# Kernel tuning notes

Hardware: AMD Instinct MI355X
Metric: run time of the kernel (lower is better)

## Reference

```python
import jax, jax.numpy as jnp
import numpy as np

N = 100000   # nodes
R = 6        # relations (edge types)
E = 400000   # edges per relation
F_IN = 128   # metapath2vec embedding dim
HID = 128    # hidden_dim (conv1 out == conv2 out in RGCN)
OUT = 2      # out_size


def setup_inputs() -> dict:
    key = jax.random.key(0)
    ks = jax.random.split(key, 9)
    x = jax.random.normal(ks[0], (N, F_IN), dtype=jnp.float32)
    edge_src = jax.random.randint(ks[1], (R, E), 0, N, dtype=jnp.int32)
    edge_dst = jax.random.randint(ks[2], (R, E), 0, N, dtype=jnp.int32)
    W1 = jax.random.normal(ks[3], (R, F_IN, HID), dtype=jnp.float32) * 0.05
    b1 = jnp.zeros((R, HID), dtype=jnp.float32)
    W2 = jax.random.normal(ks[4], (R, HID, HID), dtype=jnp.float32) * 0.05
    b2 = jnp.zeros((R, HID), dtype=jnp.float32)
    Wc = jax.random.normal(ks[5], (HID, OUT), dtype=jnp.float32) * 0.05
    bc = jnp.zeros((OUT,), dtype=jnp.float32)
    return {"x": x, "edge_src": edge_src, "edge_dst": edge_dst,
            "W1": W1, "b1": b1, "W2": W2, "b2": b2, "Wc": Wc, "bc": bc}


def _graph_conv(x, src, dst, W, b):
    """DGL GraphConv, norm='both': D_dst^{-1/2} A D_src^{-1/2} X W + b."""
    ones = jnp.ones(src.shape, x.dtype)
    deg_out = jax.ops.segment_sum(ones, src, num_segments=N)  # [N]
    deg_in = jax.ops.segment_sum(ones, dst, num_segments=N)   # [N]
    norm_src = jnp.where(deg_out > 0, jax.lax.rsqrt(jnp.maximum(deg_out, 1.0)), 0.0)
    norm_dst = jnp.where(deg_in > 0, jax.lax.rsqrt(jnp.maximum(deg_in, 1.0)), 0.0)
    msg = (x * norm_src[:, None])[src]                         # [E, F] gather
    agg = jax.ops.segment_sum(msg, dst, num_segments=N)       # [N, F] scatter-sum
    return (agg * norm_dst[:, None]) @ W + b                  # [N, H]


def _hetero_layer(x, edge_src, edge_dst, W, b):
    # HeteroGraphConv(aggregate='sum'): run each relation's GraphConv, sum results.
    conv = jax.vmap(_graph_conv, in_axes=(None, 0, 0, 0, 0))
    return conv(x, edge_src, edge_dst, W, b).sum(axis=0)      # [N, H]


def reference(x, edge_src, edge_dst, W1, b1, W2, b2, Wc, bc):
    h = jax.nn.relu(_hetero_layer(x, edge_src, edge_dst, W1, b1))
    h = _hetero_layer(h, edge_src, edge_dst, W2, b2)
    g = h.mean(axis=0)          # mean-pool node embeddings -> graph embedding
    return g @ Wc + bc          # classifier logits, shape [OUT]
```

## Files before the change

### kernel.cpp

```cpp
#include <hip/hip_runtime.h>

#define N_NODES 100000
#define NREL 6
#define NEDGE 400000
#define FDIM 128
#define HID 128

constexpr int RN = NREL * N_NODES;
constexpr int NBIN = 391;
constexpr int BINCAP = 1280;
constexpr int CSRCAP = 2304;
constexpr int CHUNK = 8192;
constexpr int NCHUNK = (NEDGE + CHUNK - 1) / CHUNK;

constexpr int NB_XC = (N_NODES * 32) / 256;
constexpr int NB_WC = (NREL * FDIM * HID) / 256;
constexpr int PREP_BLOCKS = NB_XC + NB_WC + NREL + 1;

typedef __attribute__((ext_vector_type(8))) short short8;
typedef __attribute__((ext_vector_type(4))) float f32x4;

__device__ __forceinline__ unsigned short f2bf(float f) {
  union { float f; unsigned int u; } v; v.f = f;
  unsigned int u = v.u;
  unsigned int r = (u + 0x7FFFu + ((u >> 16) & 1u)) >> 16;
  return (unsigned short)r;
}
__device__ __forceinline__ float bflo(unsigned int w) {
  union { unsigned int u; float f; } v; v.u = w << 16; return v.f;
}
__device__ __forceinline__ float bfhi(unsigned int w) {
  union { unsigned int u; float f; } v; v.u = w & 0xffff0000u; return v.f;
}

__global__ void k_zero(unsigned int* __restrict__ p, int nwords) {
  int id = blockIdx.x * blockDim.x + threadIdx.x;
  if (id < nwords) p[id] = 0u;
}

__global__ __launch_bounds__(256) void k_phase1(
    const int* __restrict__ src, const int* __restrict__ dst,
    int* __restrict__ gCurIn, int* __restrict__ gCurOut,
    unsigned int* __restrict__ stIn, unsigned int* __restrict__ stOut) {
  __shared__ int hIn[NBIN], hOut[NBIN], bIn[NBIN], bOut[NBIN];
  const int r = blockIdx.x / NCHUNK;
  const int c = blockIdx.x % NCHUNK;
  const int t = threadIdx.x;
  for (int i = t; i < NBIN; i += 256) { hIn[i] = 0; hOut[i] = 0; }
  __syncthreads();
  const int base = c * CHUNK;
  const int lim = min(CHUNK, NEDGE - base);
  const int* __restrict__ sR = src + r * NEDGE + base;
  const int* __restrict__ dR = dst + r * NEDGE + base;
  for (int i = t; i < lim; i += 256) {
    atomicAdd(&hIn[dR[i] >> 8], 1);
    atomicAdd(&hOut[sR[i] >> 8], 1);
  }
  __syncthreads();
  for (int i = t; i < NBIN; i += 256) {
    bIn[i]  = atomicAdd(&gCurIn[r * NBIN + i], hIn[i]);
    bOut[i] = atomicAdd(&gCurOut[r * NBIN + i], hOut[i]);
    hIn[i] = 0; hOut[i] = 0;
  }
  __syncthreads();
  for (int i = t; i < lim; i += 256) {
    const int s = sR[i], d = dR[i];
    const int bi = d >> 8, bo = s >> 8;
    const int pi = bIn[bi] + atomicAdd(&hIn[bi], 1);
    const int po = bOut[bo] + atomicAdd(&hOut[bo], 1);
    if (pi < BINCAP)
      stIn[(size_t)(r * NBIN + bi) * BINCAP + pi] = ((unsigned)(d & 255) << 17) | (unsigned)s;
    if (po < BINCAP)
      stOut[(size_t)(r * NBIN + bo) * BINCAP + po] = ((unsigned)(s & 255) << 17) | (unsigned)d;
  }
}

__global__ __launch_bounds__(256) void k_p2a(const unsigned int* __restrict__ stOut,
                                             const int* __restrict__ gCurOut,
                                             float* __restrict__ ns) {
  __shared__ int cnt[256];
  const int rb = blockIdx.x;
  const int r = rb / NBIN, b = rb % NBIN;
  const int t = threadIdx.x;
  cnt[t] = 0;
  __syncthreads();
  const int m = min(gCurOut[rb], BINCAP);
  const unsigned int* __restrict__ st = stOut + (size_t)rb * BINCAP;
  for (int i = t; i < m; i += 256) atomicAdd(&cnt[st[i] >> 17], 1);
  __syncthreads();
  const int n = b * 256 + t;
  if (n < N_NODES) ns[r * N_NODES + n] = cnt[t] > 0 ? rsqrtf((float)cnt[t]) : 0.f;
}

__global__ __launch_bounds__(256) void k_p2in(const unsigned int* __restrict__ stIn,
                                              const int* __restrict__ gCurIn,
                                              const float* __restrict__ ns,
                                              int4* __restrict__ meta,
                                              float* __restrict__ ndA,
                                              int2* __restrict__ csr) {
  __shared__ int cnt[256], offs[256];
  __shared__ int wsum[4];
  const int rb = blockIdx.x;
  const int r = rb / NBIN, b = rb % NBIN;
  const int t = threadIdx.x;
  cnt[t] = 0;
  __syncthreads();
  const int m = min(gCurIn[rb], BINCAP);
  const unsigned int* __restrict__ st = stIn + (size_t)rb * BINCAP;
  for (int i = t; i < m; i += 256) atomicAdd(&cnt[st[i] >> 17], 1);
  __syncthreads();
  const int lane = t & 63, wid = t >> 6;
  const int pc = (cnt[t] + 3) & ~3;
  int sum = pc;
#pragma unroll
  for (int o = 1; o < 64; o <<= 1) {
    int y = __shfl_up(sum, o);
    if (lane >= o) sum += y;
  }
  if (lane == 63) wsum[wid] = sum;
  __syncthreads();
  int wadd = 0;
  for (int w = 0; w < wid; ++w) wadd += wsum[w];
  offs[t] = sum - pc + wadd;
  __syncthreads();
  const int n = b * 256 + t;
  const int binBase = rb * CSRCAP;
  if (n < N_NODES) {
    const int d = cnt[t];
    const float nd = d > 0 ? rsqrtf((float)d) : 0.f;
    meta[r * N_NODES + n] = make_int4(d, binBase + offs[t], __float_as_int(nd), 0);
    ndA[r * N_NODES + n] = nd;
    int2* __restrict__ c = csr + binBase + offs[t];
    for (int e = d; e < ((d + 3) & ~3); ++e) c[e] = make_int2(0, 0);
  }
  __syncthreads();
  cnt[t] = 0;
  __syncthreads();
  const float* __restrict__ nsr = ns + r * N_NODES;
  for (int i = t; i < m; i += 256) {
    const unsigned int v = st[i];
    const int local = v >> 17;
    const int s = v & 0x1FFFF;
    const int pos = offs[local] + atomicAdd(&cnt[local], 1);
    csr[binBase + pos] = make_int2(s, __float_as_int(nsr[s]));
  }
}

__global__ __launch_bounds__(256) void k_p2b(const unsigned int* __restrict__ stOut,
                                             const int* __restrict__ gCurOut,
                                             const float* __restrict__ ns,
                                             const float* __restrict__ ndA,
                                             float* __restrict__ wmv) {
  __shared__ float fc[256];
  const int rb = blockIdx.x;
  const int r = rb / NBIN, b = rb % NBIN;
  const int t = threadIdx.x;
  fc[t] = 0.f;
  __syncthreads();
  const int m = min(gCurOut[rb], BINCAP);
  const unsigned int* __restrict__ st = stOut + (size_t)rb * BINCAP;
  const float* __restrict__ ndr = ndA + r * N_NODES;
  for (int i = t; i < m; i += 256) {
    const unsigned int v = st[i];
    atomicAdd(&fc[v >> 17], ndr[v & 0x1FFFF]);
  }
  __syncthreads();
  const int n = b * 256 + t;
  if (n < N_NODES) {
    const int rn = r * N_NODES + n;
    wmv[rn] = fc[t] * ns[rn];
  }
}

__global__ __launch_bounds__(256) void k_prep(
    const float* __restrict__ x, unsigned short* __restrict__ xb,
    const float* __restrict__ W1, const float* __restrict__ b1,
    const float* __restrict__ b2,
    unsigned short* __restrict__ W1T, float* __restrict__ bias1,
    float* __restrict__ bias2,
    const float* __restrict__ W2, const float* __restrict__ Wc,
    float* __restrict__ u) {
  const int b = blockIdx.x;
  const int t = threadIdx.x;
  if (b < NB_XC) {
    const int id = b * 256 + t;
    const float4 v = ((const float4*)x)[id];
    ushort4 o;
    o.x = f2bf(v.x); o.y = f2bf(v.y); o.z = f2bf(v.z); o.w = f2bf(v.w);
    ((ushort4*)xb)[id] = o;
  } else if (b < NB_XC + NB_WC) {
    const int id = (b - NB_XC) * 256 + t;
    const int r = id >> 14;
    const int rem = id & 16383;
    const int j = rem >> 7;
    const int k = rem & 127;
    W1T[id] = f2bf(W1[r * 16384 + k * 128 + j]);
  } else if (b < NB_XC + NB_WC + NREL) {
    const int r = b - (NB_XC + NB_WC);
    const int k = t >> 1;
    const int c = t & 1;
    const float* __restrict__ row = W2 + r * (HID * HID) + k * HID;
    float s = 0.f;
#pragma unroll 8
    for (int j = 0; j < HID; ++j) s = fmaf(row[j], Wc[j * 2 + c], s);
    u[(r * HID + k) * 2 + c] = s;
  } else {
    if (t < HID) {
      float s1 = 0.f, s2 = 0.f;
      for (int r = 0; r < NREL; ++r) {
        s1 += b1[r * HID + t];
        s2 += b2[r * HID + t];
      }
      bias1[t] = s1;
      bias2[t] = s2;
    }
  }
}

__global__ __launch_bounds__(256, 6) void k_layer1(
    const unsigned short* __restrict__ xb,
    const int2* __restrict__ csr_ew,
    const int4* __restrict__ meta,
    const unsigned short* __restrict__ W1T,
    const float* __restrict__ bias1,
    unsigned short* __restrict__ h)
{
  __shared__ unsigned short zA[4][16][136];
  const int tid = threadIdx.x;
  const int wave = tid >> 6;
  const int lane = tid & 63;
  const int sub = lane >> 4;
  const int flane = lane & 15;
  const int wnb = blockIdx.x * 64 + wave * 16;

  f32x4 acc[8];
#pragma unroll
  for (int t = 0; t < 8; ++t) acc[t] = (f32x4){0.f, 0.f, 0.f, 0.f};

  const int pn = wnb + flane;
  const bool pok = pn < N_NODES;
  const int pnc = pok ? pn : (N_NODES - 1);
  int4 mt = meta[pnc];
  if (!pok) { mt.x = 0; mt.z = 0; }

  for (int r = 0; r < NREL; ++r) {
#pragma unroll
    for (int pass = 0; pass < 4; ++pass) {
      const int row = pass * 4 + sub;
      const int d = __shfl(mt.x, row);
      const int o = __shfl(mt.y, row);
      const float nd = __int_as_float(__shfl(mt.z, row));
      const uint4* __restrict__ lst = (const uint4*)(csr_ew + o);
      const unsigned fo = (unsigned)(flane << 3);
      float b[8];
#pragma unroll
      for (int k = 0; k < 8; ++k) b[k] = 0.f;
      const int nb = (d + 3) >> 2;
      for (int bi = 0; bi < nb; ++bi) {
        const uint4 qa = lst[2 * bi];
        const uint4 qb = lst[2 * bi + 1];
        const float w0 = __uint_as_float(qa.y);
        const float w1 = __uint_as_float(qa.w);
        const float w2 = __uint_as_float(qb.y);
        const float w3 = __uint_as_float(qb.w);
        const uint4 v0 = *(const uint4*)(xb + ((size_t)qa.x << 7) + fo);
        const uint4 v1 = *(const uint4*)(xb + ((size_t)qa.z << 7) + fo);
        const uint4 v2 = *(const uint4*)(xb + ((size_t)qb.x << 7) + fo);
        const uint4 v3 = *(const uint4*)(xb + ((size_t)qb.z << 7) + fo);
#define ACC8(V, W) \
        b[0] = fmaf(bflo(V.x), W, b[0]); b[1] = fmaf(bfhi(V.x), W, b[1]); \
        b[2] = fmaf(bflo(V.y), W, b[2]); b[3] = fmaf(bfhi(V.y), W, b[3]); \
        b[4] = fmaf(bflo(V.z), W, b[4]); b[5] = fmaf(bfhi(V.z), W, b[5]); \
        b[6] = fmaf(bflo(V.w), W, b[6]); b[7] = fmaf(bfhi(V.w), W, b[7]);
        ACC8(v0, w0) ACC8(v1, w1) ACC8(v2, w2) ACC8(v3, w3)
#undef ACC8
      }
      uint4 pk;
      pk.x = (unsigned)f2bf(b[0] * nd) | ((unsigned)f2bf(b[1] * nd) << 16);
      pk.y = (unsigned)f2bf(b[2] * nd) | ((unsigned)f2bf(b[3] * nd) << 16);
      pk.z = (unsigned)f2bf(b[4] * nd) | ((unsigned)f2bf(b[5] * nd) << 16);
      pk.w = (unsigned)f2bf(b[6] * nd) | ((unsigned)f2bf(b[7] * nd) << 16);
      *(uint4*)(&zA[wave][row][flane * 8]) = pk;
    }
    int4 mtn = mt;
    if (r + 1 < NREL) {
      mtn = meta[(r + 1) * N_NODES + pnc];
      if (!pok) { mtn.x = 0; mtn.z = 0; }
    }
    const int m = lane & 15;
    const int qq = lane >> 4;
    const unsigned short* __restrict__ wr = W1T + r * (FDIM * HID);
#pragma unroll
    for (int kk = 0; kk < 4; ++kk) {
      const short8 af = *(const short8*)(&zA[wave][m][kk * 32 + qq * 8]);
#pragma unroll
      for (int t = 0; t < 8; ++t) {
        const short8 bfr = *(const short8*)(wr + (t * 16 + m) * 128 + kk * 32 + qq * 8);
        acc[t] = __builtin_amdgcn_mfma_f32_16x16x32_bf16(af, bfr, acc[t], 0, 0, 0);
      }
    }
    mt = mtn;
  }
  const int col = lane & 15;
  const int rq = (lane >> 4) * 4;
#pragma unroll
  for (int t = 0; t < 8; ++t) {
#pragma unroll
    for (int rr = 0; rr < 4; ++rr) {
      const int node = wnb + rq + rr;
      if (node < N_NODES) {
        const int f = t * 16 + col;
        float v = acc[t][rr] + bias1[f];
        v = fmaxf(v, 0.f);
        h[(size_t)node * FDIM + f] = f2bf(v);
      }
    }
  }
}

__global__ __launch_bounds__(256) void k_mv(const unsigned short* __restrict__ h,
                                            const float* __restrict__ wmv,
                                            float* __restrict__ mv) {
  __shared__ float sh[16][136];
  const int sub = threadIdx.x >> 4;
  const int flane = threadIdx.x & 15;
  const unsigned fo = (unsigned)(flane << 3);
  float acc[NREL][8];
#pragma unroll
  for (int r = 0; r < NREL; ++r)
#pragma unroll
    for (int k = 0; k < 8; ++k) acc[r][k] = 0.f;
  const int nbase = blockIdx.x * 256 + sub * 16;
  for (int i = 0; i < 16; ++i) {
    const int n = nbase + i;
    if (n >= N_NODES) break;
    const uint4 hv = *(const uint4*)(h + ((size_t)n << 7) + fo);
    float hf[8];
    hf[0] = bflo(hv.x); hf[1] = bfhi(hv.x); hf[2] = bflo(hv.y); hf[3] = bfhi(hv.y);
    hf[4] = bflo(hv.z); hf[5] = bfhi(hv.z); hf[6] = bflo(hv.w); hf[7] = bfhi(hv.w);
#pragma unroll
    for (int r = 0; r < NREL; ++r) {
      const float w = wmv[r * N_NODES + n];
#pragma unroll
      for (int k = 0; k < 8; ++k) acc[r][k] = fmaf(w, hf[k], acc[r][k]);
    }
  }
  const float inv = 1.0f / (float)N_NODES;
  const int t = threadIdx.x;
#pragma unroll
  for (int r = 0; r < NREL; ++r) {
    __syncthreads();
#pragma unroll
    for (int k = 0; k < 8; ++k) sh[sub][flane * 8 + k] = acc[r][k];
    __syncthreads();
    if (t < 128) {
      float s = 0.f;
#pragma unroll
      for (int j = 0; j < 16; ++j) s += sh[j][t];
      atomicAdd(&mv[r * HID + t], s * inv);
    }
  }
}

__global__ __launch_bounds__(256) void k_final(const float* __restrict__ mv,
                                               const float* __restrict__ u,
                                               const float* __restrict__ bias2,
                                               const float* __restrict__ Wc,
                                               const float* __restrict__ bc,
                                               float* __restrict__ out) {
  __shared__ float r0[256], r1[256];
  const int t = threadIdx.x;
  float s0 = 0.f, s1 = 0.f;
  for (int rk = t; rk < NREL * HID; rk += 256) {
    const float m = mv[rk];
    s0 = fmaf(m, u[rk * 2], s0);
    s1 = fmaf(m, u[rk * 2 + 1], s1);
  }
  r0[t] = s0; r1[t] = s1;
  __syncthreads();
  for (int off = 128; off > 0; off >>= 1) {
    if (t < off) { r0[t] += r0[t + off]; r1[t] += r1[t + off]; }
    __syncthreads();
  }
  if (t == 0) {
    float t0 = bc[0], t1 = bc[1];
    for (int j = 0; j < HID; ++j) {
      const float b = bias2[j];
      t0 = fmaf(b, Wc[j * 2], t0);
      t1 = fmaf(b, Wc[j * 2 + 1], t1);
    }
    out[0] = r0[0] + t0;
    out[1] = r1[0] + t1;
  }
}

extern "C" void kernel_launch(void* const* d_in, const int* in_sizes, int n_in,
                              void* d_out, int out_size, void* d_ws, size_t ws_size,
                              hipStream_t stream) {
  (void)in_sizes; (void)n_in; (void)out_size; (void)ws_size;
  const float* x   = (const float*)d_in[0];
  const int* esrc  = (const int*)d_in[1];
  const int* edst  = (const int*)d_in[2];
  const float* W1  = (const float*)d_in[3];
  const float* b1  = (const float*)d_in[4];
  const float* W2  = (const float*)d_in[5];
  const float* b2  = (const float*)d_in[6];
  const float* Wc  = (const float*)d_in[7];
  const float* bc  = (const float*)d_in[8];
  float* out = (float*)d_out;

  char* p = (char*)d_ws;
  size_t off = 0;
  auto take = [&](size_t bytes) -> void* {
    void* q = p + off;
    off += (bytes + 255) & ~(size_t)255;
    return q;
  };
  int*   gCurIn  = (int*)take((size_t)NREL * NBIN * 4);
  int*   gCurOut = (int*)take((size_t)NREL * NBIN * 4);
  float* mv      = (float*)take((size_t)NREL * HID * 4);
  const size_t zero_bytes = off;
  float* ns   = (float*)take((size_t)RN * 4);
  float* ndA  = (float*)take((size_t)RN * 4);
  float* wmv  = (float*)take((size_t)RN * 4);
  int4*  meta = (int4*)take((size_t)RN * 16);
  unsigned int* stIn  = (unsigned int*)take((size_t)NREL * NBIN * BINCAP * 4);
  unsigned int* stOut = (unsigned int*)take((size_t)NREL * NBIN * BINCAP * 4);
  int2* csr = (int2*)take((size_t)NREL * NBIN * CSRCAP * 8);
  unsigned short* W1T = (unsigned short*)take((size_t)NREL * FDIM * HID * 2);
  float* bias1 = (float*)take(HID * 4);
  float* bias2 = (float*)take(HID * 4);
  float* u     = (float*)take((size_t)NREL * HID * 2 * 4);
  unsigned short* h  = (unsigned short*)take((size_t)N_NODES * FDIM * 2);
  unsigned short* xb = (unsigned short*)take((size_t)N_NODES * FDIM * 2);

  const int zero_words = (int)(zero_bytes / 4);
  k_zero<<<(zero_words + 255) / 256, 256, 0, stream>>>((unsigned int*)d_ws, zero_words);
  k_phase1<<<NREL * NCHUNK, 256, 0, stream>>>(esrc, edst, gCurIn, gCurOut, stIn, stOut);
  k_p2a<<<NREL * NBIN, 256, 0, stream>>>(stOut, gCurOut, ns);
  k_p2in<<<NREL * NBIN, 256, 0, stream>>>(stIn, gCurIn, ns, meta, ndA, csr);
  k_p2b<<<NREL * NBIN, 256, 0, stream>>>(stOut, gCurOut, ns, ndA, wmv);
  k_prep<<<PREP_BLOCKS, 256, 0, stream>>>(x, xb, W1, b1, b2, W1T, bias1, bias2, W2, Wc, u);
  k_layer1<<<(N_NODES + 63) / 64, 256, 0, stream>>>(xb, csr, meta, W1T, bias1, h);
  k_mv<<<(N_NODES + 255) / 256, 256, 0, stream>>>(h, wmv, mv);
  k_final<<<1, 256, 0, stream>>>(mv, u, bias2, Wc, bc, out);
}
```

Measured before the change: 590.2 us.

## Interleave four node gathers per lane with prefetched edge lists in layer1

Layer-1 aggregation now runs the four rows each lane group handles together, looping to the group's max degree with masked zero-weight loads. The next edge-list block is prefetched while the current features are accumulated, which raises memory-level parallelism for the irregular gathers. The output is staged through shared memory so h is written with coalesced 16-byte stores instead of scattered 2-byte ones. The cost is more registers, reflected in launch bounds relaxed from 6 to 2 blocks per CU, and wasted masked gathers when degrees are uneven.

```diff
diff --git a/kernel.cpp b/kernel.cpp
--- a/kernel.cpp
+++ b/kernel.cpp
@@ -217,7 +217,7 @@
   }
 }
 
-__global__ __launch_bounds__(256, 6) void k_layer1(
+__global__ __launch_bounds__(256, 2) void k_layer1(
     const unsigned short* __restrict__ xb,
     const int2* __restrict__ csr_ew,
     const int4* __restrict__ meta,
@@ -243,43 +243,90 @@
   int4 mt = meta[pnc];
   if (!pok) { mt.x = 0; mt.z = 0; }
 
+  const unsigned fo = (unsigned)(flane << 3);
+
   for (int r = 0; r < NREL; ++r) {
-#pragma unroll
-    for (int pass = 0; pass < 4; ++pass) {
-      const int row = pass * 4 + sub;
-      const int d = __shfl(mt.x, row);
-      const int o = __shfl(mt.y, row);
-      const float nd = __int_as_float(__shfl(mt.z, row));
-      const uint4* __restrict__ lst = (const uint4*)(csr_ew + o);
-      const unsigned fo = (unsigned)(flane << 3);
-      float b[8];
-#pragma unroll
-      for (int k = 0; k < 8; ++k) b[k] = 0.f;
-      const int nb = (d + 3) >> 2;
-      for (int bi = 0; bi < nb; ++bi) {
-        const uint4 qa = lst[2 * bi];
-        const uint4 qb = lst[2 * bi + 1];
-        const float w0 = __uint_as_float(qa.y);
-        const float w1 = __uint_as_float(qa.w);
-        const float w2 = __uint_as_float(qb.y);
-        const float w3 = __uint_as_float(qb.w);
-        const uint4 v0 = *(const uint4*)(xb + ((size_t)qa.x << 7) + fo);
-        const uint4 v1 = *(const uint4*)(xb + ((size_t)qa.z << 7) + fo);
-        const uint4 v2 = *(const uint4*)(xb + ((size_t)qb.x << 7) + fo);
-        const uint4 v3 = *(const uint4*)(xb + ((size_t)qb.z << 7) + fo);
+    int d4[4], o4[4];
+    float nd4[4];
+#pragma unroll
+    for (int p = 0; p < 4; ++p) {
+      const int row = p * 4 + sub;
+      d4[p] = __shfl(mt.x, row);
+      o4[p] = __shfl(mt.y, row);
+      nd4[p] = __int_as_float(__shfl(mt.z, row));
+    }
+    int dmax = mt.x;
+#pragma unroll
+    for (int s = 8; s >= 1; s >>= 1) dmax = max(dmax, __shfl_xor(dmax, s));
+    const int nbmax = (dmax + 3) >> 2;
+
+    float b[4][8];
+#pragma unroll
+    for (int p = 0; p < 4; ++p)
+#pragma unroll
+      for (int k = 0; k < 8; ++k) b[p][k] = 0.f;
+
+    uint4 qa[4], qb[4];
+#pragma unroll
+    for (int p = 0; p < 4; ++p) {
+      const uint4* __restrict__ lst = (const uint4*)(csr_ew + o4[p]);
+      qa[p] = lst[0];
+      qb[p] = lst[1];
+    }
+
+    for (int bi = 0; bi < nbmax; ++bi) {
+      float w0[4], w1[4], w2[4], w3[4];
+      unsigned a0[4], a1[4], a2[4], a3[4];
+#pragma unroll
+      for (int p = 0; p < 4; ++p) {
+        const bool act = bi < ((d4[p] + 3) >> 2);
+        w0[p] = act ? __uint_as_float(qa[p].y) : 0.f;
+        w1[p] = act ? __uint_as_float(qa[p].w) : 0.f;
+        w2[p] = act ? __uint_as_float(qb[p].y) : 0.f;
+        w3[p] = act ? __uint_as_float(qb[p].w) : 0.f;
+        a0[p] = act ? (((unsigned)qa[p].x << 7) + fo) : fo;
+        a1[p] = act ? (((unsigned)qa[p].z << 7) + fo) : fo;
+        a2[p] = act ? (((unsigned)qb[p].x << 7) + fo) : fo;
+        a3[p] = act ? (((unsigned)qb[p].z << 7) + fo) : fo;
+      }
+      uint4 v0[4], v1[4], v2[4], v3[4];
+#pragma unroll
+      for (int p = 0; p < 4; ++p) {
+        v0[p] = *(const uint4*)(xb + a0[p]);
+        v1[p] = *(const uint4*)(xb + a1[p]);
+        v2[p] = *(const uint4*)(xb + a2[p]);
+        v3[p] = *(const uint4*)(xb + a3[p]);
+      }
+#pragma unroll
+      for (int p = 0; p < 4; ++p) {
+        const int nb_p = (d4[p] + 3) >> 2;
+        const int bn = bi + 1;
+        const int qoff = o4[p] + ((bn < nb_p) ? (bn << 2) : 0);
+        const uint4* __restrict__ lst = (const uint4*)(csr_ew + qoff);
+        qa[p] = lst[0];
+        qb[p] = lst[1];
+      }
+#pragma unroll
+      for (int p = 0; p < 4; ++p) {
 #define ACC8(V, W) \
-        b[0] = fmaf(bflo(V.x), W, b[0]); b[1] = fmaf(bfhi(V.x), W, b[1]); \
-        b[2] = fmaf(bflo(V.y), W, b[2]); b[3] = fmaf(bfhi(V.y), W, b[3]); \
-        b[4] = fmaf(bflo(V.z), W, b[4]); b[5] = fmaf(bfhi(V.z), W, b[5]); \
-        b[6] = fmaf(bflo(V.w), W, b[6]); b[7] = fmaf(bfhi(V.w), W, b[7]);
-        ACC8(v0, w0) ACC8(v1, w1) ACC8(v2, w2) ACC8(v3, w3)
+        b[p][0] = fmaf(bflo(V.x), W, b[p][0]); b[p][1] = fmaf(bfhi(V.x), W, b[p][1]); \
+        b[p][2] = fmaf(bflo(V.y), W, b[p][2]); b[p][3] = fmaf(bfhi(V.y), W, b[p][3]); \
+        b[p][4] = fmaf(bflo(V.z), W, b[p][4]); b[p][5] = fmaf(bfhi(V.z), W, b[p][5]); \
+        b[p][6] = fmaf(bflo(V.w), W, b[p][6]); b[p][7] = fmaf(bfhi(V.w), W, b[p][7]);
+        ACC8(v0[p], w0[p]) ACC8(v1[p], w1[p]) ACC8(v2[p], w2[p]) ACC8(v3[p], w3[p])
 #undef ACC8
       }
+    }
+
+#pragma unroll
+    for (int p = 0; p < 4; ++p) {
+      const int row = p * 4 + sub;
+      const float nd = nd4[p];
       uint4 pk;
-      pk.x = (unsigned)f2bf(b[0] * nd) | ((unsigned)f2bf(b[1] * nd) << 16);
-      pk.y = (unsigned)f2bf(b[2] * nd) | ((unsigned)f2bf(b[3] * nd) << 16);
-      pk.z = (unsigned)f2bf(b[4] * nd) | ((unsigned)f2bf(b[5] * nd) << 16);
-      pk.w = (unsigned)f2bf(b[6] * nd) | ((unsigned)f2bf(b[7] * nd) << 16);
+      pk.x = (unsigned)f2bf(b[p][0] * nd) | ((unsigned)f2bf(b[p][1] * nd) << 16);
+      pk.y = (unsigned)f2bf(b[p][2] * nd) | ((unsigned)f2bf(b[p][3] * nd) << 16);
+      pk.z = (unsigned)f2bf(b[p][4] * nd) | ((unsigned)f2bf(b[p][5] * nd) << 16);
+      pk.w = (unsigned)f2bf(b[p][6] * nd) | ((unsigned)f2bf(b[p][7] * nd) << 16);
       *(uint4*)(&zA[wave][row][flane * 8]) = pk;
     }
     int4 mtn = mt;
@@ -301,19 +348,26 @@
     }
     mt = mtn;
   }
+
   const int col = lane & 15;
   const int rq = (lane >> 4) * 4;
 #pragma unroll
   for (int t = 0; t < 8; ++t) {
+    const float bsv = bias1[t * 16 + col];
 #pragma unroll
     for (int rr = 0; rr < 4; ++rr) {
-      const int node = wnb + rq + rr;
-      if (node < N_NODES) {
-        const int f = t * 16 + col;
-        float v = acc[t][rr] + bias1[f];
-        v = fmaxf(v, 0.f);
-        h[(size_t)node * FDIM + f] = f2bf(v);
-      }
+      float v = acc[t][rr] + bsv;
+      v = fmaxf(v, 0.f);
+      zA[wave][rq + rr][t * 16 + col] = f2bf(v);
+    }
+  }
+#pragma unroll
+  for (int rr2 = 0; rr2 < 4; ++rr2) {
+    const int row = rr2 * 4 + sub;
+    const int node = wnb + row;
+    if (node < N_NODES) {
+      const uint4 hv = *(const uint4*)(&zA[wave][row][flane * 8]);
+      *(uint4*)(h + ((size_t)node << 7) + fo) = hv;
     }
   }
 }
```

New measurement: 514.2 us, median of 2. -12.9%, faster.
